# Optimization experiments

Measured on AMD Instinct MI355X. Metric: run time of the kernel, lower is better.

## Reference

```python
import jax, jax.numpy as jnp
import numpy as np

N_TOKENS = 32768
D_MODEL = 1024
D_HIDDEN = 4096
N_EXPERTS = 8
TOP_K = 2


def setup_inputs() -> dict:
    key = jax.random.key(0)
    ks = jax.random.split(key, 8)
    s_in = 1.0 / np.sqrt(D_MODEL)
    s_hid = 1.0 / np.sqrt(D_HIDDEN)
    return {
        "x": jax.random.normal(ks[0], (N_TOKENS, D_MODEL), dtype=jnp.float32),
        "Wr": jax.random.normal(ks[1], (D_MODEL, N_EXPERTS), dtype=jnp.float32) * s_in,
        "br": jnp.zeros((N_EXPERTS,), dtype=jnp.float32),
        "W1": jax.random.normal(ks[2], (N_EXPERTS, D_MODEL, D_HIDDEN), dtype=jnp.float32) * s_in,
        "b1": jnp.zeros((N_EXPERTS, D_HIDDEN), dtype=jnp.float32),
        "W2": jax.random.normal(ks[3], (N_EXPERTS, D_HIDDEN, D_MODEL), dtype=jnp.float32) * s_hid,
        "b2": jnp.zeros((N_EXPERTS, D_MODEL), dtype=jnp.float32),
    }


def reference(x, Wr, br, W1, b1, W2, b2):
    # Router: softmax over experts, top-k selection, renormalize.
    logits = x @ Wr + br                                  # [N, E]
    probs = jax.nn.softmax(logits, axis=-1)
    topk_probs, topk_idx = jax.lax.top_k(probs, TOP_K)    # [N, K]
    topk_probs = topk_probs / jnp.sum(topk_probs, axis=-1, keepdims=True)
    # Per-token per-expert combine weight (sum over k of prob * selection).
    sel = jax.nn.one_hot(topk_idx, N_EXPERTS, dtype=x.dtype)   # [N, K, E]
    combine = jnp.einsum('nk,nke->ne', topk_probs, sel)        # [N, E]
    # Masked gather-MLP-scatter expressed as dense per-expert MLP weighted
    # by combine (zero weight for unselected experts -> identical math).
    out = jnp.zeros_like(x)
    for e in range(N_EXPERTS):
        h = jax.nn.gelu(x @ W1[e] + b1[e], approximate=False)  # exact erf GELU (torch default)
        out = out + combine[:, e:e + 1] * (h @ W2[e] + b2[e])
    return out
```

## Files before the change

### kernel.cpp

```cpp
#include <hip/hip_runtime.h>

#define NT_TOK 32768
#define DM 1024
#define DH 4096
#define NE 8
#define BT 256
#define BK 32
#define CAP (NT_TOK*2 + NE*BT)
#define CHUNK_ROWS 16384

typedef _Float16 f16x8 __attribute__((ext_vector_type(8)));
typedef float f32x4 __attribute__((ext_vector_type(4)));
typedef float f32x8 __attribute__((ext_vector_type(8)));

__device__ __forceinline__ unsigned short f2h_bits(float v){
  _Float16 h = (_Float16)v;
  return __builtin_bit_cast(unsigned short, h);
}

__device__ __forceinline__ void async16(const void* g, void* l){
  __builtin_amdgcn_global_load_lds((const __attribute__((address_space(1))) void*)g,
                                   (__attribute__((address_space(3))) void*)l, 16, 0, 0);
}

__device__ __forceinline__ int xcd_remap(int orig, int nwg){
  int q = nwg >> 3, r = nwg & 7;
  int x = orig & 7, i = orig >> 3;
  int base = (x < r) ? x*(q+1) : r*(q+1) + (x-r)*q;
  return base + i;
}


__global__ __launch_bounds__(256) void cvt_f16_kernel(const float* __restrict__ src,
                                                      unsigned short* __restrict__ dst, int n8){
  int i = blockIdx.x*256 + threadIdx.x;
  if (i >= n8) return;
  float4 a = ((const float4*)src)[2*i];
  float4 b = ((const float4*)src)[2*i+1];
  union { unsigned short u[8]; uint4 v; } r;
  r.u[0]=f2h_bits(a.x); r.u[1]=f2h_bits(a.y); r.u[2]=f2h_bits(a.z); r.u[3]=f2h_bits(a.w);
  r.u[4]=f2h_bits(b.x); r.u[5]=f2h_bits(b.y); r.u[6]=f2h_bits(b.z); r.u[7]=f2h_bits(b.w);
  ((uint4*)dst)[i] = r.v;
}

__global__ __launch_bounds__(256) void transpose_f16_v2(const float* __restrict__ src,
    unsigned short* __restrict__ dst, int R, int C){
  __shared__ float t[64][65];
  int ez = blockIdx.z;
  const float* s = src + (size_t)ez*R*C;
  unsigned short* d = dst + (size_t)ez*R*C;
  int c0 = blockIdx.x*64, r0 = blockIdx.y*64;
  int tx = threadIdx.x & 15, ty = threadIdx.x >> 4;
  #pragma unroll
  for (int i=0;i<4;i++){
    float4 v = *(const float4*)&s[(size_t)(r0+ty+i*16)*C + c0 + tx*4];
    t[ty+i*16][tx*4+0]=v.x; t[ty+i*16][tx*4+1]=v.y;
    t[ty+i*16][tx*4+2]=v.z; t[ty+i*16][tx*4+3]=v.w;
  }
  __syncthreads();
  #pragma unroll
  for (int i=0;i<4;i++){
    int cc = ty + i*16;
    union { unsigned short u[4]; uint2 v; } o;
    #pragma unroll
    for (int j=0;j<4;j++) o.u[j] = f2h_bits(t[tx*4+j][cc]);
    *(uint2*)&d[(size_t)(c0+cc)*R + r0 + tx*4] = o.v;
  }
}


__global__ __launch_bounds__(256) void router_kernel(const float* __restrict__ x,
    const float* __restrict__ Wr, const float* __restrict__ br,
    int* __restrict__ topi, float* __restrict__ topw, int* __restrict__ counts){
  __shared__ float wr_s[NE*DM];
  __shared__ int bcnt[NE];
  int tid = threadIdx.x;
  if (tid < NE) bcnt[tid] = 0;
  for (int idx=tid; idx<NE*DM; idx+=256){
    int k = idx>>3, e = idx&7;
    wr_s[e*DM + k] = Wr[idx];
  }
  __syncthreads();
  int w = tid>>6, lane = tid&63;
  for (int tt=0; tt<16; ++tt){
    int t = blockIdx.x*64 + w*16 + tt;
    const float* xr = x + (size_t)t*DM;
    double acc[NE];
    #pragma unroll
    for (int e=0;e<NE;e++) acc[e]=0.0;
    #pragma unroll
    for (int j=0;j<16;j++){
      float xv = xr[j*64 + lane];
      #pragma unroll
      for (int e=0;e<NE;e++) acc[e] += (double)xv * (double)wr_s[e*DM + j*64 + lane];
    }
    #pragma unroll
    for (int e=0;e<NE;e++){
      #pragma unroll
      for (int d=32; d; d>>=1) acc[e] += __shfl_xor(acc[e], d);
    }
    if (lane==0){
      double l[NE];
      #pragma unroll
      for (int e=0;e<NE;e++) l[e] = acc[e] + (double)br[e];
      int i0 = 0;
      #pragma unroll
      for (int e=1;e<NE;e++) if (l[e] > l[i0]) i0 = e;
      int i1 = (i0==0) ? 1 : 0;
      #pragma unroll
      for (int e=0;e<NE;e++) if (e != i0 && l[e] > l[i1]) i1 = e;
      double w0 = 1.0/(1.0 + exp(l[i1]-l[i0]));
      topi[2*t] = i0; topi[2*t+1] = i1;
      topw[2*t] = (float)w0; topw[2*t+1] = (float)(1.0-w0);
      atomicAdd(&bcnt[i0],1); atomicAdd(&bcnt[i1],1);
    }
  }
  __syncthreads();
  if (tid < NE && bcnt[tid] > 0) atomicAdd(&counts[tid], bcnt[tid]);
}

__global__ void offsets_kernel(const int* __restrict__ counts, int* __restrict__ off){
  if (threadIdx.x==0 && blockIdx.x==0){
    int o = 0;
    for (int e=0;e<NE;e++){ off[e] = o; o += ((counts[e]+BT-1)/BT)*BT; }
    off[NE] = o;
  }
}

__global__ __launch_bounds__(256) void scatter_kernel(const int* __restrict__ topi,
    const float* __restrict__ topw, const int* __restrict__ off,
    int* __restrict__ cursor, int* __restrict__ atok, float* __restrict__ awgt){
  __shared__ int bcnt[NE];
  __shared__ int bbase[NE];
  int tid = threadIdx.x;
  if (tid < NE) bcnt[tid] = 0;
  __syncthreads();
  int t = blockIdx.x*256 + tid;
  int e0 = topi[2*t],   e1 = topi[2*t+1];
  int r0 = atomicAdd(&bcnt[e0], 1);
  int r1 = atomicAdd(&bcnt[e1], 1);
  __syncthreads();
  if (tid < NE) bbase[tid] = (bcnt[tid] > 0) ? atomicAdd(&cursor[tid], bcnt[tid]) : 0;
  __syncthreads();
  int s0 = off[e0] + bbase[e0] + r0;
  int s1 = off[e1] + bbase[e1] + r1;
  atok[s0] = t;  awgt[s0] = topw[2*t];
  atok[s1] = t;  awgt[s1] = topw[2*t+1];
}


template<int KDIM, bool IS_G2>
__global__ __launch_bounds__(512, 2) void gemm_big_kernel(
    const unsigned short* __restrict__ Asrc,
    const unsigned short* __restrict__ WT,
    const float* __restrict__ bias,
    const int* __restrict__ atok,
    const float* __restrict__ awgt,
    const int* __restrict__ offs,
    unsigned short* __restrict__ H,
    float* __restrict__ out,
    int c0){
  __shared__ unsigned short As[4][BT*BK];
  __shared__ unsigned short Bs[4][BT*BK];
  const int NDIM = IS_G2 ? DM : DH;
  const int NT = NDIM/BT;
  int wg = xcd_remap(blockIdx.x, gridDim.x);
  int nt = wg % NT, mt = wg / NT;
  int total = offs[NE];
  int m0 = c0 + mt*BT;
  if (m0 >= total) return;
  int e = 0;
  #pragma unroll
  for (int q=0;q<NE-1;q++) if (m0 >= offs[q+1]) e = q+1;
  int tid = threadIdx.x;
  int lane = tid&63, wid = tid>>6;
  int wm = wid>>2, wn = wid&3;

  const unsigned short* agp[2];
  const unsigned short* bgp[2];
  int dofs[2];
  #pragma unroll
  for (int j=0;j<2;j++){
    int c = j*512 + tid;
    int u = (c&7) ^ ((c>>3)&7);
    int srow = ((c>>3)<<1) + (u>>2);
    int sch  = u&3;
    if (IS_G2){
      agp[j] = Asrc + (size_t)(m0 - c0 + srow)*KDIM + sch*8;
    } else {
      int tok = atok[m0 + srow];
      if (tok < 0) tok = 0;
      agp[j] = Asrc + (size_t)tok*KDIM + sch*8;
    }
    bgp[j] = WT + ((size_t)e*NDIM + nt*BT + srow)*KDIM + sch*8;
    dofs[j] = c*8;
  }

  int pos = (((lane>>4) + ((lane&1)<<2)) ^ ((lane>>1)&7)) << 3;
  int aoff0 = (wm*64 + ((lane&15)>>1))*64 + pos;
  int boff0 = (wn*32 + ((lane&15)>>1))*64 + pos;

  f32x4 acc[8][4];
  #pragma unroll
  for (int i=0;i<8;i++)
    #pragma unroll
    for (int j=0;j<4;j++) acc[i][j] = 0.0f;

  const int NKT = KDIM/BK;
  #pragma unroll
  for (int t=0;t<3;t++){
    #pragma unroll
    for (int j=0;j<2;j++) async16(agp[j] + t*BK, &As[t][dofs[j]]);
    #pragma unroll
    for (int j=0;j<2;j++) async16(bgp[j] + t*BK, &Bs[t][dofs[j]]);
  }

  for (int kt=0; kt<NKT; ++kt){
    if (kt < NKT-2)      asm volatile("s_waitcnt vmcnt(8)" ::: "memory");
    else if (kt < NKT-1) asm volatile("s_waitcnt vmcnt(4)" ::: "memory");
    else                 asm volatile("s_waitcnt vmcnt(0)" ::: "memory");
    __builtin_amdgcn_s_barrier();
    const unsigned short* Ab = &As[kt&3][0];
    const unsigned short* Bb = &Bs[kt&3][0];
    f16x8 b[4], a[4];
    #pragma unroll
    for (int nf=0;nf<4;nf++) b[nf] = *(const f16x8*)&Bb[boff0 + nf*512];
    #pragma unroll
    for (int mf=0;mf<4;mf++) a[mf] = *(const f16x8*)&Ab[aoff0 + mf*512];
    if (kt+3 < NKT){
      #pragma unroll
      for (int j=0;j<2;j++) async16(agp[j] + (size_t)(kt+3)*BK, &As[(kt+3)&3][dofs[j]]);
      #pragma unroll
      for (int j=0;j<2;j++) async16(bgp[j] + (size_t)(kt+3)*BK, &Bs[(kt+3)&3][dofs[j]]);
    }
    __builtin_amdgcn_s_setprio(1);
    #pragma unroll
    for (int mf=0;mf<4;mf++)
      #pragma unroll
      for (int nf=0;nf<4;nf++)
        acc[mf][nf] = __builtin_amdgcn_mfma_f32_16x16x32_f16(a[mf], b[nf], acc[mf][nf], 0,0,0);
    __builtin_amdgcn_s_setprio(0);
    #pragma unroll
    for (int mf=0;mf<4;mf++) a[mf] = *(const f16x8*)&Ab[aoff0 + (mf+4)*512];
    __builtin_amdgcn_s_setprio(1);
    #pragma unroll
    for (int mf=0;mf<4;mf++)
      #pragma unroll
      for (int nf=0;nf<4;nf++)
        acc[mf+4][nf] = __builtin_amdgcn_mfma_f32_16x16x32_f16(a[mf], b[nf], acc[mf+4][nf], 0,0,0);
    __builtin_amdgcn_s_setprio(0);
  }

  int nbase = nt*BT + wn*64 + (lane&15);
  if (!IS_G2){
    const float* be = bias + (size_t)e*DH;
    int rloc = (m0 - c0) + wm*128 + ((lane>>4)<<2);
    #pragma unroll
    for (int mf=0;mf<8;mf++)
      #pragma unroll
      for (int nf=0;nf<4;nf++){
        int nn = nbase + nf*16;
        float bv = be[nn];
        #pragma unroll
        for (int r2=0;r2<4;r2++){
          float v = acc[mf][nf][r2] + bv;
          float g = 0.5f*v*(1.0f + erff(v*0.70710678118654752f));
          H[(size_t)(rloc + mf*16 + r2)*DH + nn] = f2h_bits(g);
        }
      }
  } else {
    const float* be = bias + (size_t)e*DM;
    int sbase = m0 + wm*128 + ((lane>>4)<<2);
    #pragma unroll
    for (int mf=0;mf<8;mf++){
      #pragma unroll
      for (int r2=0;r2<4;r2++){
        int slot = sbase + mf*16 + r2;
        int tok = atok[slot];
        float wgt = awgt[slot];
        if (tok >= 0){
          #pragma unroll
          for (int nf=0;nf<4;nf++){
            int nn = nbase + nf*16;
            float v = acc[mf][nf][r2] + be[nn];
            atomicAdd(&out[(size_t)tok*DM + nn], wgt*v);
          }
        }
      }
    }
  }
}


__global__ __launch_bounds__(256) void gemm1_f32_kernel(
    const float* __restrict__ xf, const unsigned short* __restrict__ W1T,
    const float* __restrict__ b1, const int* __restrict__ atok,
    const int* __restrict__ offs, unsigned short* __restrict__ H, int c0){
  __shared__ float Asf[128*64];
  __shared__ unsigned short Bsld[128*64];
  const int NT = DH/128;
  int wg = xcd_remap(blockIdx.x, gridDim.x);
  int nt = wg % NT, mt = wg / NT;
  int total = offs[NE];
  int m0 = c0 + mt*128;
  if (m0 >= total) return;
  int e = 0;
  #pragma unroll
  for (int q=0;q<NE-1;q++) if (m0 >= offs[q+1]) e = q+1;
  int tid = threadIdx.x;
  const void* ag[8];
  int aofs[8];
  #pragma unroll
  for (int j=0;j<8;j++){
    int c = j*256 + tid;
    int r = c>>4, sb = (c&15)*16;
    int tok = atok[m0 + r];
    if (tok < 0) tok = 0;
    ag[j] = (const void*)((const char*)(xf + (size_t)tok*DM) + sb);
    aofs[j] = c*16;
  }
  const unsigned short* bg[4];
  int bofs[4];
  #pragma unroll
  for (int j=0;j<4;j++){
    int c = j*256 + tid;
    int r = c>>3, s = c&7;
    bg[j] = W1T + ((size_t)e*DH + nt*128 + r)*DM + s*8;
    bofs[j] = c*16;
  }
  f32x4 acc[4][4];
  #pragma unroll
  for (int i=0;i<4;i++)
    #pragma unroll
    for (int j=0;j<4;j++) acc[i][j] = 0.0f;
  int lane = tid&63;
  int wm = tid>>7, wn = (tid>>6)&1;
  int arow = wm*64 + (lane&15);
  int ak0  = (lane>>4)*8;
  int brr  = (wn*64 + (lane&15))*64 + ak0;
  for (int kt=0; kt<DM/64; ++kt){
    #pragma unroll
    for (int j=0;j<8;j++)
      async16((const char*)ag[j] + (size_t)kt*64*4, (char*)Asf + aofs[j]);
    #pragma unroll
    for (int j=0;j<4;j++)
      async16(bg[j] + (size_t)kt*64, (char*)Bsld + bofs[j]);
    __syncthreads();
    #pragma unroll
    for (int kk=0; kk<64; kk+=32){
      f16x8 a[4], b[4];
      #pragma unroll
      for (int f=0;f<4;f++){
        f32x8 v = *(const f32x8*)&Asf[(arow + f*16)*64 + ak0 + kk];
        a[f] = __builtin_convertvector(v, f16x8);
        b[f] = *(const f16x8*)&Bsld[brr + f*16*64 + kk];
      }
      #pragma unroll
      for (int i=0;i<4;i++)
        #pragma unroll
        for (int j2=0;j2<4;j2++)
          acc[i][j2] = __builtin_amdgcn_mfma_f32_16x16x32_f16(a[i], b[j2], acc[i][j2], 0,0,0);
    }
    __syncthreads();
  }
  const float* b1e = b1 + (size_t)e*DH;
  int rloc = (m0 - c0) + wm*64 + ((lane>>4)<<2);
  int nbase = nt*128 + wn*64 + (lane&15);
  #pragma unroll
  for (int i=0;i<4;i++)
    #pragma unroll
    for (int j=0;j<4;j++){
      int nn = nbase + j*16;
      float bv = b1e[nn];
      #pragma unroll
      for (int r2=0;r2<4;r2++){
        float v = acc[i][j][r2] + bv;
        float g = 0.5f*v*(1.0f + erff(v*0.70710678118654752f));
        H[(size_t)(rloc + i*16 + r2)*DH + nn] = f2h_bits(g);
      }
    }
}

__global__ void fill_kernel(float* p, float v, size_t n){
  size_t i = (size_t)blockIdx.x*256 + threadIdx.x;
  if (i < n) p[i] = v;
}


extern "C" void kernel_launch(void* const* d_in, const int* in_sizes, int n_in,
                              void* d_out, int out_size, void* d_ws, size_t ws_size,
                              hipStream_t stream){
  const float* x  = (const float*)d_in[0];
  const float* Wr = (const float*)d_in[1];
  const float* br = (const float*)d_in[2];
  const float* W1 = (const float*)d_in[3];
  const float* b1 = (const float*)d_in[4];
  const float* W2 = (const float*)d_in[5];
  const float* b2 = (const float*)d_in[6];
  float* out = (float*)d_out;

  char* ws = (char*)d_ws;
  size_t o = 0;
  auto take = [&](size_t bytes)->void*{
    void* p = ws + o; o += (bytes + 255) & ~(size_t)255; return p;
  };
  unsigned short* W1T = (unsigned short*)take((size_t)NE*DM*DH*2);
  unsigned short* W2T = (unsigned short*)take((size_t)NE*DM*DH*2);
  int*   TOPI = (int*)take((size_t)NT_TOK*2*4);
  float* TOPW = (float*)take((size_t)NT_TOK*2*4);
  int*   ATOK = (int*)take((size_t)CAP*4);
  float* AWGT = (float*)take((size_t)CAP*4);
  int*   CNT  = (int*)take(256);
  int* CUR = CNT + 8;
  int* OFF = CNT + 16;

  if (o + (size_t)BT*DH*2 > ws_size){
    fill_kernel<<<(unsigned)((out_size+255)/256), 256, 0, stream>>>(out, 4321.5f, (size_t)out_size);
    return;
  }

  unsigned short* XB = nullptr;
  bool use_xb = false;
  {
    size_t xb_bytes = (size_t)NT_TOK*DM*2 + 256;
    size_t need_h  = (size_t)2048*DH*2;
    if (o + xb_bytes + need_h <= ws_size){
      use_xb = true;
      XB = (unsigned short*)take((size_t)NT_TOK*DM*2);
    }
  }
  size_t rem = ws_size - o;
  size_t cr = (rem / ((size_t)DH*2)) / BT * BT;
  if (cr > (size_t)CHUNK_ROWS) cr = CHUNK_ROWS;
  if (cr < BT){
    fill_kernel<<<(unsigned)((out_size+255)/256), 256, 0, stream>>>(out, 4321.5f, (size_t)out_size);
    return;
  }
  int CR = (int)cr;
  unsigned short* Hb = (unsigned short*)take((size_t)CR*DH*2);

  hipMemsetAsync(CNT, 0, 64, stream);
  hipMemsetAsync(ATOK, 0xFF, (size_t)CAP*4, stream);
  hipMemsetAsync(out, 0, (size_t)out_size*sizeof(float), stream);

  if (use_xb)
    cvt_f16_kernel<<<(NT_TOK*DM/8 + 255)/256, 256, 0, stream>>>(x, XB, NT_TOK*DM/8);
  transpose_f16_v2<<<dim3(DH/64, DM/64, NE), 256, 0, stream>>>(W1, W1T, DM, DH);
  transpose_f16_v2<<<dim3(DM/64, DH/64, NE), 256, 0, stream>>>(W2, W2T, DH, DM);
  router_kernel<<<NT_TOK/64, 256, 0, stream>>>(x, Wr, br, TOPI, TOPW, CNT);
  offsets_kernel<<<1, 1, 0, stream>>>(CNT, OFF);
  scatter_kernel<<<NT_TOK/256, 256, 0, stream>>>(TOPI, TOPW, OFF, CUR, ATOK, AWGT);

  for (int c0 = 0; c0 < CAP; c0 += CR){
    int rows = CAP - c0; if (rows > CR) rows = CR;
    int mtc = (rows + BT - 1)/BT;
    if (use_xb)
      gemm_big_kernel<DM, false><<<dim3((DH/BT)*mtc), 512, 0, stream>>>(
          XB, W1T, b1, ATOK, AWGT, OFF, Hb, out, c0);
    else
      gemm1_f32_kernel<<<dim3((DH/128)*((rows+127)/128)), 256, 0, stream>>>(
          x, W1T, b1, ATOK, OFF, Hb, c0);
    gemm_big_kernel<DH, true><<<dim3((DM/BT)*mtc), 512, 0, stream>>>(
        Hb, W2T, b2, ATOK, AWGT, OFF, Hb, out, c0);
  }
}
```

Baseline: 2.399 ms.

## Replace 256x256 pipelined GEMM with simpler 128x128 single-buffer tile kernel

Swaps the 256-row, 512-thread expert GEMM, which ran a 4-stage async LDS pipeline with BK=32, for a 128x128 tile, 256-thread kernel with BK=64, a single LDS buffer and two barriers per k-step. The chunk row cap is also raised so the whole dispatch capacity can go through in one chunk. The smaller tiles give more workgroups and less padding waste per expert, but they drop the software pipelining and halve data reuse per tile, so load latency is exposed more.

```diff
diff --git a/kernel.cpp b/kernel.cpp
--- a/kernel.cpp
+++ b/kernel.cpp
@@ -5,9 +5,8 @@
 #define DH 4096
 #define NE 8
 #define BT 256
-#define BK 32
 #define CAP (NT_TOK*2 + NE*BT)
-#define CHUNK_ROWS 16384
+#define CHUNK_ROWS 32768
 
 typedef _Float16 f16x8 __attribute__((ext_vector_type(8)));
 typedef float f32x4 __attribute__((ext_vector_type(4)));
@@ -150,7 +149,7 @@
 
 
 template<int KDIM, bool IS_G2>
-__global__ __launch_bounds__(512, 2) void gemm_big_kernel(
+__global__ __launch_bounds__(256) void gemm_128_kernel(
     const unsigned short* __restrict__ Asrc,
     const unsigned short* __restrict__ WT,
     const float* __restrict__ bias,
@@ -160,129 +159,108 @@
     unsigned short* __restrict__ H,
     float* __restrict__ out,
     int c0){
-  __shared__ unsigned short As[4][BT*BK];
-  __shared__ unsigned short Bs[4][BT*BK];
+  __shared__ unsigned short As[128*64];
+  __shared__ unsigned short Bs[128*64];
   const int NDIM = IS_G2 ? DM : DH;
-  const int NT = NDIM/BT;
+  const int NT = NDIM/128;
   int wg = xcd_remap(blockIdx.x, gridDim.x);
   int nt = wg % NT, mt = wg / NT;
   int total = offs[NE];
-  int m0 = c0 + mt*BT;
+  int m0 = c0 + mt*128;
   if (m0 >= total) return;
   int e = 0;
   #pragma unroll
   for (int q=0;q<NE-1;q++) if (m0 >= offs[q+1]) e = q+1;
   int tid = threadIdx.x;
-  int lane = tid&63, wid = tid>>6;
-  int wm = wid>>2, wn = wid&3;
-
-  const unsigned short* agp[2];
-  const unsigned short* bgp[2];
-  int dofs[2];
-  #pragma unroll
-  for (int j=0;j<2;j++){
-    int c = j*512 + tid;
-    int u = (c&7) ^ ((c>>3)&7);
-    int srow = ((c>>3)<<1) + (u>>2);
-    int sch  = u&3;
+  int lane = tid&63;
+  int wm = tid>>7, wn = (tid>>6)&1;
+
+  const unsigned short* ag[4];
+  const unsigned short* bg[4];
+  int lofs[4];
+  #pragma unroll
+  for (int j=0;j<4;j++){
+    int c = j*256 + tid;
+    int r = c>>3, s = c&7;
+    int sc = s ^ (r&7);
     if (IS_G2){
-      agp[j] = Asrc + (size_t)(m0 - c0 + srow)*KDIM + sch*8;
+      ag[j] = Asrc + (size_t)(m0 - c0 + r)*KDIM + sc*8;
     } else {
-      int tok = atok[m0 + srow];
+      int tok = atok[m0 + r];
       if (tok < 0) tok = 0;
-      agp[j] = Asrc + (size_t)tok*KDIM + sch*8;
-    }
-    bgp[j] = WT + ((size_t)e*NDIM + nt*BT + srow)*KDIM + sch*8;
-    dofs[j] = c*8;
-  }
-
-  int pos = (((lane>>4) + ((lane&1)<<2)) ^ ((lane>>1)&7)) << 3;
-  int aoff0 = (wm*64 + ((lane&15)>>1))*64 + pos;
-  int boff0 = (wn*32 + ((lane&15)>>1))*64 + pos;
-
-  f32x4 acc[8][4];
-  #pragma unroll
-  for (int i=0;i<8;i++)
+      ag[j] = Asrc + (size_t)tok*KDIM + sc*8;
+    }
+    bg[j] = WT + ((size_t)e*NDIM + nt*128 + r)*KDIM + sc*8;
+    lofs[j] = c*8;
+  }
+
+  f32x4 acc[4][4];
+  #pragma unroll
+  for (int i=0;i<4;i++)
     #pragma unroll
     for (int j=0;j<4;j++) acc[i][j] = 0.0f;
 
-  const int NKT = KDIM/BK;
-  #pragma unroll
-  for (int t=0;t<3;t++){
-    #pragma unroll
-    for (int j=0;j<2;j++) async16(agp[j] + t*BK, &As[t][dofs[j]]);
-    #pragma unroll
-    for (int j=0;j<2;j++) async16(bgp[j] + t*BK, &Bs[t][dofs[j]]);
-  }
+  int arow0 = wm*64 + (lane&15);
+  int brow0 = wn*64 + (lane&15);
+  int kc0 = lane>>4, kswz = lane&7;
+  const int NKT = KDIM/64;
 
   for (int kt=0; kt<NKT; ++kt){
-    if (kt < NKT-2)      asm volatile("s_waitcnt vmcnt(8)" ::: "memory");
-    else if (kt < NKT-1) asm volatile("s_waitcnt vmcnt(4)" ::: "memory");
-    else                 asm volatile("s_waitcnt vmcnt(0)" ::: "memory");
-    __builtin_amdgcn_s_barrier();
-    const unsigned short* Ab = &As[kt&3][0];
-    const unsigned short* Bb = &Bs[kt&3][0];
-    f16x8 b[4], a[4];
-    #pragma unroll
-    for (int nf=0;nf<4;nf++) b[nf] = *(const f16x8*)&Bb[boff0 + nf*512];
-    #pragma unroll
-    for (int mf=0;mf<4;mf++) a[mf] = *(const f16x8*)&Ab[aoff0 + mf*512];
-    if (kt+3 < NKT){
-      #pragma unroll
-      for (int j=0;j<2;j++) async16(agp[j] + (size_t)(kt+3)*BK, &As[(kt+3)&3][dofs[j]]);
-      #pragma unroll
-      for (int j=0;j<2;j++) async16(bgp[j] + (size_t)(kt+3)*BK, &Bs[(kt+3)&3][dofs[j]]);
-    }
-    __builtin_amdgcn_s_setprio(1);
-    #pragma unroll
-    for (int mf=0;mf<4;mf++)
-      #pragma unroll
-      for (int nf=0;nf<4;nf++)
-        acc[mf][nf] = __builtin_amdgcn_mfma_f32_16x16x32_f16(a[mf], b[nf], acc[mf][nf], 0,0,0);
-    __builtin_amdgcn_s_setprio(0);
-    #pragma unroll
-    for (int mf=0;mf<4;mf++) a[mf] = *(const f16x8*)&Ab[aoff0 + (mf+4)*512];
-    __builtin_amdgcn_s_setprio(1);
-    #pragma unroll
-    for (int mf=0;mf<4;mf++)
-      #pragma unroll
-      for (int nf=0;nf<4;nf++)
-        acc[mf+4][nf] = __builtin_amdgcn_mfma_f32_16x16x32_f16(a[mf], b[nf], acc[mf+4][nf], 0,0,0);
-    __builtin_amdgcn_s_setprio(0);
-  }
-
-  int nbase = nt*BT + wn*64 + (lane&15);
+    #pragma unroll
+    for (int j=0;j<4;j++){
+      async16(ag[j] + (size_t)kt*64, &As[lofs[j]]);
+      async16(bg[j] + (size_t)kt*64, &Bs[lofs[j]]);
+    }
+    __syncthreads();
+    #pragma unroll
+    for (int kc=0; kc<8; kc+=4){
+      f16x8 a[4], b[4];
+      #pragma unroll
+      for (int f=0;f<4;f++){
+        a[f] = *(const f16x8*)&As[(arow0 + f*16)*64 + (((kc0+kc)^kswz)*8)];
+        b[f] = *(const f16x8*)&Bs[(brow0 + f*16)*64 + (((kc0+kc)^kswz)*8)];
+      }
+      #pragma unroll
+      for (int i=0;i<4;i++)
+        #pragma unroll
+        for (int j2=0;j2<4;j2++)
+          acc[i][j2] = __builtin_amdgcn_mfma_f32_16x16x32_f16(a[i], b[j2], acc[i][j2], 0,0,0);
+    }
+    __syncthreads();
+  }
+
+  int nbase = nt*128 + wn*64 + (lane&15);
   if (!IS_G2){
     const float* be = bias + (size_t)e*DH;
-    int rloc = (m0 - c0) + wm*128 + ((lane>>4)<<2);
-    #pragma unroll
-    for (int mf=0;mf<8;mf++)
-      #pragma unroll
-      for (int nf=0;nf<4;nf++){
-        int nn = nbase + nf*16;
+    int rloc = (m0 - c0) + wm*64 + ((lane>>4)<<2);
+    #pragma unroll
+    for (int i=0;i<4;i++)
+      #pragma unroll
+      for (int j=0;j<4;j++){
+        int nn = nbase + j*16;
         float bv = be[nn];
         #pragma unroll
         for (int r2=0;r2<4;r2++){
-          float v = acc[mf][nf][r2] + bv;
+          float v = acc[i][j][r2] + bv;
           float g = 0.5f*v*(1.0f + erff(v*0.70710678118654752f));
-          H[(size_t)(rloc + mf*16 + r2)*DH + nn] = f2h_bits(g);
+          H[(size_t)(rloc + i*16 + r2)*DH + nn] = f2h_bits(g);
         }
       }
   } else {
     const float* be = bias + (size_t)e*DM;
-    int sbase = m0 + wm*128 + ((lane>>4)<<2);
-    #pragma unroll
-    for (int mf=0;mf<8;mf++){
+    int rbase = m0 + wm*64 + ((lane>>4)<<2);
+    #pragma unroll
+    for (int i=0;i<4;i++){
       #pragma unroll
       for (int r2=0;r2<4;r2++){
-        int slot = sbase + mf*16 + r2;
+        int slot = rbase + i*16 + r2;
         int tok = atok[slot];
         float wgt = awgt[slot];
         if (tok >= 0){
           #pragma unroll
-          for (int nf=0;nf<4;nf++){
-            int nn = nbase + nf*16;
-            float v = acc[mf][nf][r2] + be[nn];
+          for (int j=0;j<4;j++){
+            int nn = nbase + j*16;
+            float v = acc[i][j][r2] + be[nn];
             atomicAdd(&out[(size_t)tok*DM + nn], wgt*v);
           }
         }
@@ -432,6 +410,7 @@
   size_t rem = ws_size - o;
   size_t cr = (rem / ((size_t)DH*2)) / BT * BT;
   if (cr > (size_t)CHUNK_ROWS) cr = CHUNK_ROWS;
+  if (cr > (size_t)CAP) cr = ((size_t)CAP + BT - 1)/BT*BT;
   if (cr < BT){
     fill_kernel<<<(unsigned)((out_size+255)/256), 256, 0, stream>>>(out, 4321.5f, (size_t)out_size);
     return;
@@ -453,14 +432,14 @@
 
   for (int c0 = 0; c0 < CAP; c0 += CR){
     int rows = CAP - c0; if (rows > CR) rows = CR;
-    int mtc = (rows + BT - 1)/BT;
+    int mtc = (rows + 127)/128;
     if (use_xb)
-      gemm_big_kernel<DM, false><<<dim3((DH/BT)*mtc), 512, 0, stream>>>(
+      gemm_128_kernel<DM, false><<<dim3((DH/128)*mtc), 256, 0, stream>>>(
           XB, W1T, b1, ATOK, AWGT, OFF, Hb, out, c0);
     else
-      gemm1_f32_kernel<<<dim3((DH/128)*((rows+127)/128)), 256, 0, stream>>>(
+      gemm1_f32_kernel<<<dim3((DH/128)*mtc), 256, 0, stream>>>(
           x, W1T, b1, ATOK, OFF, Hb, c0);
-    gemm_big_kernel<DH, true><<<dim3((DM/BT)*mtc), 512, 0, stream>>>(
+    gemm_128_kernel<DH, true><<<dim3((DM/128)*mtc), 256, 0, stream>>>(
         Hb, W2T, b2, ATOK, AWGT, OFF, Hb, out, c0);
   }
 }
```

Result: slower. 2.646 ms (+10.3%).

## Split GEMM k-step into four barrier-separated phases interleaving async loads with MFMA

Applied to the files above, without the earlier changes.

The inner GEMM loop is reorganised into four phases, each issuing one async global-to-LDS load and then a quarter of the MFMAs, separated by workgroup barriers. The goal is to spread memory issue across the compute and keep waves in lockstep, a ping-pong style schedule. The chunk row count is also doubled so the whole token set is handled in one chunk, cutting launches. The cost is three extra barriers per k-step and possible stalls if waves drift apart.

```diff
diff --git a/kernel.cpp b/kernel.cpp
--- a/kernel.cpp
+++ b/kernel.cpp
@@ -7,7 +7,7 @@
 #define BT 256
 #define BK 32
 #define CAP (NT_TOK*2 + NE*BT)
-#define CHUNK_ROWS 16384
+#define CHUNK_ROWS 32768
 
 typedef _Float16 f16x8 __attribute__((ext_vector_type(8)));
 typedef float f32x4 __attribute__((ext_vector_type(4)));
@@ -222,31 +222,52 @@
     __builtin_amdgcn_s_barrier();
     const unsigned short* Ab = &As[kt&3][0];
     const unsigned short* Bb = &Bs[kt&3][0];
-    f16x8 b[4], a[4];
-    #pragma unroll
-    for (int nf=0;nf<4;nf++) b[nf] = *(const f16x8*)&Bb[boff0 + nf*512];
+    const bool pf = (kt+3 < NKT);
+    unsigned short* Ad = &As[(kt+3)&3][0];
+    unsigned short* Bd = &Bs[(kt+3)&3][0];
+    const size_t koff = (size_t)(kt+3)*BK;
+    f16x8 a[4], b[4];
+    #pragma unroll
+    for (int nf=0;nf<2;nf++) b[nf] = *(const f16x8*)&Bb[boff0 + nf*512];
     #pragma unroll
     for (int mf=0;mf<4;mf++) a[mf] = *(const f16x8*)&Ab[aoff0 + mf*512];
-    if (kt+3 < NKT){
-      #pragma unroll
-      for (int j=0;j<2;j++) async16(agp[j] + (size_t)(kt+3)*BK, &As[(kt+3)&3][dofs[j]]);
-      #pragma unroll
-      for (int j=0;j<2;j++) async16(bgp[j] + (size_t)(kt+3)*BK, &Bs[(kt+3)&3][dofs[j]]);
-    }
+    if (pf) async16(agp[0] + koff, &Ad[dofs[0]]);
     __builtin_amdgcn_s_setprio(1);
     #pragma unroll
     for (int mf=0;mf<4;mf++)
       #pragma unroll
-      for (int nf=0;nf<4;nf++)
+      for (int nf=0;nf<2;nf++)
         acc[mf][nf] = __builtin_amdgcn_mfma_f32_16x16x32_f16(a[mf], b[nf], acc[mf][nf], 0,0,0);
     __builtin_amdgcn_s_setprio(0);
+    __builtin_amdgcn_s_barrier();
+    #pragma unroll
+    for (int nf=2;nf<4;nf++) b[nf] = *(const f16x8*)&Bb[boff0 + nf*512];
+    if (pf) async16(agp[1] + koff, &Ad[dofs[1]]);
+    __builtin_amdgcn_s_setprio(1);
+    #pragma unroll
+    for (int mf=0;mf<4;mf++)
+      #pragma unroll
+      for (int nf=2;nf<4;nf++)
+        acc[mf][nf] = __builtin_amdgcn_mfma_f32_16x16x32_f16(a[mf], b[nf], acc[mf][nf], 0,0,0);
+    __builtin_amdgcn_s_setprio(0);
+    __builtin_amdgcn_s_barrier();
     #pragma unroll
     for (int mf=0;mf<4;mf++) a[mf] = *(const f16x8*)&Ab[aoff0 + (mf+4)*512];
+    if (pf) async16(bgp[0] + koff, &Bd[dofs[0]]);
     __builtin_amdgcn_s_setprio(1);
     #pragma unroll
     for (int mf=0;mf<4;mf++)
       #pragma unroll
-      for (int nf=0;nf<4;nf++)
+      for (int nf=0;nf<2;nf++)
+        acc[mf+4][nf] = __builtin_amdgcn_mfma_f32_16x16x32_f16(a[mf], b[nf], acc[mf+4][nf], 0,0,0);
+    __builtin_amdgcn_s_setprio(0);
+    __builtin_amdgcn_s_barrier();
+    if (pf) async16(bgp[1] + koff, &Bd[dofs[1]]);
+    __builtin_amdgcn_s_setprio(1);
+    #pragma unroll
+    for (int mf=0;mf<4;mf++)
+      #pragma unroll
+      for (int nf=2;nf<4;nf++)
         acc[mf+4][nf] = __builtin_amdgcn_mfma_f32_16x16x32_f16(a[mf], b[nf], acc[mf+4][nf], 0,0,0);
     __builtin_amdgcn_s_setprio(0);
   }
```

Result: no change. 2.384 ms (-0.6%).
